# Performance work log

Measured on AMD Instinct MI355X. Metric: run time of the kernel, lower is better.

The kernel has to match this reference:

```python
import jax, jax.numpy as jnp
import numpy as np

B, C, IMG, P = 32, 3, 224, 16
D, L, H, EXP, NCLS = 768, 12, 12, 4, 1000
NP = (IMG // P) ** 2        # 196 patches
N = NP + 1                  # 197 tokens with cls
DH = D // H                 # 64 head dim
EPS = 1e-5


def setup_inputs() -> dict:
    key = jax.random.key(0)
    ks = iter(jax.random.split(key, 32))
    s = 0.02
    return {
        "img": jax.random.normal(next(ks), (B, C, IMG, IMG), jnp.float32),
        "patch_w": jax.random.normal(next(ks), (D, C * P * P), jnp.float32) * s,
        "patch_b": jnp.zeros((D,), jnp.float32),
        "cls_token": jax.random.normal(next(ks), (D,), jnp.float32) * s,
        "pos_emb": jax.random.normal(next(ks), (N, D), jnp.float32) * s,
        "ln1_w": jnp.ones((L, D), jnp.float32),
        "ln1_b": jnp.zeros((L, D), jnp.float32),
        "qkv_w": jax.random.normal(next(ks), (L, 3 * D, D), jnp.float32) * s,
        "qkv_b": jnp.zeros((L, 3 * D), jnp.float32),
        "proj_w": jax.random.normal(next(ks), (L, D, D), jnp.float32) * s,
        "proj_b": jnp.zeros((L, D), jnp.float32),
        "ln2_w": jnp.ones((L, D), jnp.float32),
        "ln2_b": jnp.zeros((L, D), jnp.float32),
        "ff1_w": jax.random.normal(next(ks), (L, EXP * D, D), jnp.float32) * s,
        "ff1_b": jnp.zeros((L, EXP * D), jnp.float32),
        "ff2_w": jax.random.normal(next(ks), (L, D, EXP * D), jnp.float32) * s,
        "ff2_b": jnp.zeros((L, D), jnp.float32),
        "head1_w": jax.random.normal(next(ks), (EXP * D, D), jnp.float32) * s,
        "head1_b": jnp.zeros((EXP * D,), jnp.float32),
        "head2_w": jax.random.normal(next(ks), (NCLS, EXP * D), jnp.float32) * s,
        "head2_b": jnp.zeros((NCLS,), jnp.float32),
    }


def _ln(x, w, b):
    m = x.mean(-1, keepdims=True)
    v = ((x - m) ** 2).mean(-1, keepdims=True)
    return (x - m) * jax.lax.rsqrt(v + EPS) * w + b


def _vit(img, patch_w, patch_b, cls_token, pos_emb, ln1_w, ln1_b, qkv_w, qkv_b,
         proj_w, proj_b, ln2_w, ln2_b, ff1_w, ff1_b, ff2_w, ff2_b,
         head1_w, head1_b, head2_w, head2_b):
    b = img.shape[0]
    g = IMG // P
    # Rearrange 'b c (h p1) (w p2) -> b (h w) (p1 p2 c)'
    x = img.reshape(b, C, g, P, g, P)
    x = x.transpose(0, 2, 4, 3, 5, 1).reshape(b, g * g, P * P * C)
    tokens = x @ patch_w.T + patch_b                           # [B, NP, D]
    cls = jnp.broadcast_to(cls_token, (b, 1, D))
    tokens = jnp.concatenate([cls, tokens], axis=1) + pos_emb  # [B, N, D]

    scale = DH ** -0.5

    def block(x, p):
        l1w, l1b, qw, qb, pw, pb, l2w, l2b, f1w, f1b, f2w, f2b = p
        h = _ln(x, l1w, l1b)
        qkv = h @ qw.T + qb                                    # [B, N, 3D]
        # '(h d qkv)' factorization: heads outermost, qkv innermost
        qkv = qkv.reshape(b, N, H, DH, 3).transpose(4, 0, 2, 1, 3)
        q, k, v = qkv[0], qkv[1], qkv[2]                       # [B, H, N, DH]
        scores = jnp.einsum('bhqd,bhkd->bhqk', q, k) * scale
        attn = jnp.einsum('bhqk,bhkd->bhqd', jax.nn.softmax(scores, axis=-1), v)
        attn = attn.transpose(0, 2, 1, 3).reshape(b, N, D)
        x = x + attn @ pw.T + pb
        h = _ln(x, l2w, l2b)
        h = jax.nn.gelu(h @ f1w.T + f1b, approximate=False)
        x = x + h @ f2w.T + f2b
        return x, None

    params = (ln1_w, ln1_b, qkv_w, qkv_b, proj_w, proj_b,
              ln2_w, ln2_b, ff1_w, ff1_b, ff2_w, ff2_b)
    tokens, _ = jax.lax.scan(block, tokens, params)

    latent = tokens[:, 0]                                      # [B, D]
    h = jnp.tanh(latent @ head1_w.T + head1_b)
    return h @ head2_w.T + head2_b                             # [B, NCLS]


def reference(img, patch_w, patch_b, cls_token, pos_emb, ln1_w, ln1_b, qkv_w,
              qkv_b, proj_w, proj_b, ln2_w, ln2_b, ff1_w, ff1_b, ff2_w, ff2_b,
              head1_w, head1_b, head2_w, head2_b):
    return _vit(img, patch_w, patch_b, cls_token, pos_emb, ln1_w, ln1_b,
                qkv_w, qkv_b, proj_w, proj_b, ln2_w, ln2_b, ff1_w, ff1_b,
                ff2_w, ff2_b, head1_w, head1_b, head2_w, head2_b)
```

## Files before the change

### kernel.cpp

```cpp
#include <hip/hip_runtime.h>
#include <math.h>

typedef unsigned short u16;
using bf16x8 = __attribute__((ext_vector_type(8))) short;
using f32x4  = __attribute__((ext_vector_type(4))) float;

#define DEV __device__ __forceinline__

constexpr int Bc = 32, Cc = 3, IMGc = 224, Pc = 16, Dc = 768, Lc = 12, Hc = 12, NCLSc = 1000;
constexpr int NPc = 196, Nc = 197, DHc = 64;
constexpr int M0 = Bc * Nc;
constexpr int MP = 6400;
constexpr int MPATCH = Bc * NPc;
constexpr int NKP = 224;
constexpr int NB = Bc * Hc;

DEV u16 f2b(float f) { union { float f; unsigned u; } c; c.f = f; unsigned r = c.u + 0x7fffu + ((c.u >> 16) & 1u); return (u16)(r >> 16); }
DEV float b2f(u16 b) { union { float f; unsigned u; } c; c.u = ((unsigned)b) << 16; return c.f; }

DEV float wsum(float v) {
#pragma unroll
  for (int m = 32; m >= 1; m >>= 1) v += __shfl_xor(v, m, 64);
  return v;
}
DEV float wmax(float v) {
#pragma unroll
  for (int m = 32; m >= 1; m >>= 1) v = fmaxf(v, __shfl_xor(v, m, 64));
  return v;
}

DEV void load_lds16(const u16* g, u16* l) {
  __builtin_amdgcn_global_load_lds((const __attribute__((address_space(1))) void*)g,
                                   (__attribute__((address_space(3))) void*)l, 16, 0, 0);
}


__global__ void cvt_kern(const float* __restrict__ in, u16* __restrict__ out, long n4) {
  long i = (long)blockIdx.x * 256 + threadIdx.x;
  if (i >= n4) return;
  float4 v = ((const float4*)in)[i];
  ushort4 r;
  r.x = f2b(v.x); r.y = f2b(v.y); r.z = f2b(v.z); r.w = f2b(v.w);
  ((ushort4*)out)[i] = r;
}

__global__ void patchify_kern(const float* __restrict__ img, u16* __restrict__ Xp) {
  int i = blockIdx.x * 256 + threadIdx.x;
  if (i >= MPATCH * Dc) return;
  int r = i / Dc, f = i - r * Dc;
  int b = r / NPc, g = r - b * NPc;
  int gi = g / 14, gj = g - gi * 14;
  int c = f % 3, t2 = f / 3;
  int pj = t2 & 15, pi = t2 >> 4;
  float v = img[(((long)(b * 3 + c) * 224) + gi * 16 + pi) * 224 + gj * 16 + pj];
  Xp[i] = f2b(v);
}

__global__ void addpos_kern(float* __restrict__ x, const float* __restrict__ cls, const float* __restrict__ pos) {
  int i = blockIdx.x * 256 + threadIdx.x;
  if (i >= M0 * 192) return;
  int row = i / 192, q = i - row * 192;
  int n = row % Nc;
  float4 p = ((const float4*)pos)[n * 192 + q];
  float4* dst = (float4*)x + (long)row * 192 + q;
  if (n == 0) {
    float4 cv = ((const float4*)cls)[q];
    float4 o; o.x = cv.x + p.x; o.y = cv.y + p.y; o.z = cv.z + p.z; o.w = cv.w + p.w;
    *dst = o;
  } else {
    float4 o = *dst;
    o.x += p.x; o.y += p.y; o.z += p.z; o.w += p.w;
    *dst = o;
  }
}

__global__ __launch_bounds__(256) void ln_kern(const float* __restrict__ x, const float* __restrict__ w,
                                               const float* __restrict__ b, u16* __restrict__ out, int rows) {
  int wid = threadIdx.x >> 6, l = threadIdx.x & 63;
  int row = blockIdx.x * 4 + wid;
  if (row >= rows) return;
  const float4* xr = (const float4*)(x + (long)row * Dc);
  float4 v[3];
#pragma unroll
  for (int i = 0; i < 3; ++i) v[i] = xr[i * 64 + l];
  float s = 0;
#pragma unroll
  for (int i = 0; i < 3; ++i) s += v[i].x + v[i].y + v[i].z + v[i].w;
  s = wsum(s);
  float mean = s * (1.0f / Dc);
  float ss = 0;
#pragma unroll
  for (int i = 0; i < 3; ++i) {
    float a0 = v[i].x - mean, a1 = v[i].y - mean, a2 = v[i].z - mean, a3 = v[i].w - mean;
    ss += a0 * a0 + a1 * a1 + a2 * a2 + a3 * a3;
  }
  ss = wsum(ss);
  float rs = rsqrtf(ss * (1.0f / Dc) + 1e-5f);
  const float4* w4 = (const float4*)w;
  const float4* b4 = (const float4*)b;
#pragma unroll
  for (int i = 0; i < 3; ++i) {
    int pos = i * 64 + l;
    float4 wv = w4[pos], bv = b4[pos];
    ushort4 o;
    o.x = f2b((v[i].x - mean) * rs * wv.x + bv.x);
    o.y = f2b((v[i].y - mean) * rs * wv.y + bv.y);
    o.z = f2b((v[i].z - mean) * rs * wv.z + bv.z);
    o.w = f2b((v[i].w - mean) * rs * wv.w + bv.w);
    ((ushort4*)out)[(long)row * 192 + pos] = o;
  }
}

__global__ __launch_bounds__(256) void softmax_kern(u16* __restrict__ S) {
  int wid = threadIdx.x >> 6, l = threadIdx.x & 63;
  int q = blockIdx.x * 4 + wid;
  if (q >= Nc) return;
  int z = blockIdx.y;
  u16* rowp = S + ((long)z * NKP + q) * NKP;
  float vals[4];
  float mx = -1e30f;
#pragma unroll
  for (int i = 0; i < 4; ++i) {
    int col = i * 64 + l;
    float vv = (col < Nc) ? b2f(rowp[col]) : -1e30f;
    vals[i] = vv;
    mx = fmaxf(mx, vv);
  }
  mx = wmax(mx);
  float sum = 0;
#pragma unroll
  for (int i = 0; i < 4; ++i) {
    int col = i * 64 + l;
    float e = (col < Nc) ? expf(vals[i] - mx) : 0.f;
    vals[i] = e;
    sum += e;
  }
  sum = wsum(sum);
  float inv = 1.0f / sum;
#pragma unroll
  for (int i = 0; i < 4; ++i) {
    int col = i * 64 + l;
    if (col < NKP) rowp[col] = (col < Nc) ? f2b(vals[i] * inv) : (u16)0;
  }
}

__global__ void latent_kern(const float* __restrict__ x, u16* __restrict__ lat) {
  int i = blockIdx.x * 256 + threadIdx.x;
  if (i >= Bc * Dc) return;
  int b = i / Dc, d = i - b * Dc;
  lat[i] = f2b(x[(long)(b * Nc) * Dc + d]);
}


enum { EPI_F32 = 0, EPI_PATCH, EPI_BF16, EPI_PV, EPI_RES, EPI_GELU, EPI_TANH, EPI_QKV };

struct GP {
  const u16* A; const u16* W;
  int lda, ldb, ldc;
  long sA, sW, sC;
  int K;
  int Aclamp, Wclamp;
  int Mv, Nv;
  float alpha;
  const float* bias;
  float* Cf; u16* Cb;
  u16 *q, *k, *v;
};

template <int EPI>
__global__ __launch_bounds__(256) void gemm_bt(GP p) {
  __shared__ alignas(16) u16 As[128 * 32];
  __shared__ alignas(16) u16 Ws[128 * 32];
  const int z = blockIdx.z;
  const u16* Ab = p.A + (long)z * p.sA;
  const u16* Wb = p.W + (long)z * p.sW;
  const int tid = threadIdx.x;
  const int l = tid & 63, wid = tid >> 6;
  const int quad = l >> 4, lr = l & 15;
  const int wr = wid >> 1, wc = wid & 1;
  const int tm = blockIdx.y * 128, tn = blockIdx.x * 128;

  f32x4 acc[4][4];
  f32x4 z4 = {0.f, 0.f, 0.f, 0.f};
#pragma unroll
  for (int i = 0; i < 4; ++i)
#pragma unroll
    for (int j = 0; j < 4; ++j) acc[i][j] = z4;

  const int sr = tid >> 2;
  const int sc = (tid & 3) * 8;
  const int ar0 = min(tm + sr, p.Aclamp - 1);
  const int ar1 = min(tm + 64 + sr, p.Aclamp - 1);
  const int wrr0 = min(tn + sr, p.Wclamp - 1);
  const int wrr1 = min(tn + 64 + sr, p.Wclamp - 1);
  const u16* a0 = Ab + (long)ar0 * p.lda + sc;
  const u16* a1 = Ab + (long)ar1 * p.lda + sc;
  const u16* w0 = Wb + (long)wrr0 * p.ldb + sc;
  const u16* w1 = Wb + (long)wrr1 * p.ldb + sc;

  for (int k0 = 0; k0 < p.K; k0 += 32) {
    load_lds16(a0 + k0, &As[tid * 8]);
    load_lds16(a1 + k0, &As[2048 + tid * 8]);
    load_lds16(w0 + k0, &Ws[tid * 8]);
    load_lds16(w1 + k0, &Ws[2048 + tid * 8]);
    __syncthreads();
    bf16x8 af[4], wf[4];
#pragma unroll
    for (int mi = 0; mi < 4; ++mi) af[mi] = *(const bf16x8*)&As[(wr * 64 + mi * 16 + lr) * 32 + quad * 8];
#pragma unroll
    for (int ni = 0; ni < 4; ++ni) wf[ni] = *(const bf16x8*)&Ws[(wc * 64 + ni * 16 + lr) * 32 + quad * 8];
#pragma unroll
    for (int mi = 0; mi < 4; ++mi)
#pragma unroll
      for (int ni = 0; ni < 4; ++ni)
        acc[mi][ni] = __builtin_amdgcn_mfma_f32_16x16x32_bf16(af[mi], wf[ni], acc[mi][ni], 0, 0, 0);
    __syncthreads();
  }

  if constexpr (EPI == EPI_QKV) {
    int hh[4], dh[4], ss[4]; float bv[4];
#pragma unroll
    for (int ni = 0; ni < 4; ++ni) {
      int col = tn + wc * 64 + ni * 16 + lr;
      hh[ni] = col / 192;
      int rem = col - hh[ni] * 192;
      dh[ni] = rem / 3;
      ss[ni] = rem - 3 * dh[ni];
      bv[ni] = p.bias[col];
    }
#pragma unroll
    for (int mi = 0; mi < 4; ++mi)
#pragma unroll
      for (int j = 0; j < 4; ++j) {
        int row = tm + wr * 64 + mi * 16 + quad * 4 + j;
        if (row >= p.Mv) continue;
        int b = row / Nc, n = row - Nc * b;
#pragma unroll
        for (int ni = 0; ni < 4; ++ni) {
          float val = acc[mi][ni][j] + bv[ni];
          if (ss[ni] == 0) {
            val *= p.alpha;
            p.q[(((long)(b * Hc + hh[ni])) * Nc + n) * DHc + dh[ni]] = f2b(val);
          } else if (ss[ni] == 1) {
            p.k[(((long)(b * Hc + hh[ni])) * Nc + n) * DHc + dh[ni]] = f2b(val);
          } else {
            p.v[(((long)(b * Hc + hh[ni])) * DHc + dh[ni]) * NKP + n] = f2b(val);
          }
        }
      }
  } else {
#pragma unroll
    for (int mi = 0; mi < 4; ++mi)
#pragma unroll
      for (int j = 0; j < 4; ++j) {
        int row = tm + wr * 64 + mi * 16 + quad * 4 + j;
        if (row >= p.Mv) continue;
#pragma unroll
        for (int ni = 0; ni < 4; ++ni) {
          int col = tn + wc * 64 + ni * 16 + lr;
          if (col >= p.Nv) continue;
          float val = acc[mi][ni][j];
          if constexpr (EPI == EPI_F32) {
            p.Cf[(long)z * p.sC + (long)row * p.ldc + col] = val + p.bias[col];
          }
          if constexpr (EPI == EPI_PATCH) {
            int b = row / NPc, t = row - NPc * b;
            p.Cf[((long)(b * Nc + 1 + t)) * p.ldc + col] = val + p.bias[col];
          }
          if constexpr (EPI == EPI_BF16) {
            p.Cb[(long)z * p.sC + (long)row * p.ldc + col] = f2b(val);
          }
          if constexpr (EPI == EPI_PV) {
            long off = (long)(z / Hc) * (Nc * Dc) + (long)(z % Hc) * DHc;
            p.Cb[off + (long)row * Dc + col] = f2b(val);
          }
          if constexpr (EPI == EPI_RES) {
            long ix = (long)row * p.ldc + col;
            p.Cf[ix] += val + p.bias[col];
          }
          if constexpr (EPI == EPI_GELU) {
            float t2 = val + p.bias[col];
            p.Cb[(long)row * p.ldc + col] = f2b(0.5f * t2 * (1.0f + erff(t2 * 0.70710678118f)));
          }
          if constexpr (EPI == EPI_TANH) {
            float t2 = val + p.bias[col];
            p.Cb[(long)row * p.ldc + col] = f2b(tanhf(t2));
          }
        }
      }
  }
}


static void cvt(const float* in, u16* out, long n, hipStream_t s) {
  long n4 = n / 4;
  cvt_kern<<<dim3((unsigned)((n4 + 255) / 256)), dim3(256), 0, s>>>(in, out, n4);
}

extern "C" void kernel_launch(void* const* d_in, const int* in_sizes, int n_in,
                              void* d_out, int out_size, void* d_ws, size_t ws_size,
                              hipStream_t stream) {
  const float* img     = (const float*)d_in[0];
  const float* patch_w = (const float*)d_in[1];
  const float* patch_b = (const float*)d_in[2];
  const float* cls_tok = (const float*)d_in[3];
  const float* pos_emb = (const float*)d_in[4];
  const float* ln1_w   = (const float*)d_in[5];
  const float* ln1_b   = (const float*)d_in[6];
  const float* qkv_w   = (const float*)d_in[7];
  const float* qkv_b   = (const float*)d_in[8];
  const float* proj_w  = (const float*)d_in[9];
  const float* proj_b  = (const float*)d_in[10];
  const float* ln2_w   = (const float*)d_in[11];
  const float* ln2_b   = (const float*)d_in[12];
  const float* ff1_w   = (const float*)d_in[13];
  const float* ff1_b   = (const float*)d_in[14];
  const float* ff2_w   = (const float*)d_in[15];
  const float* ff2_b   = (const float*)d_in[16];
  const float* h1_w    = (const float*)d_in[17];
  const float* h1_b    = (const float*)d_in[18];
  const float* h2_w    = (const float*)d_in[19];
  const float* h2_b    = (const float*)d_in[20];
  float* out = (float*)d_out;

  char* ws = (char*)d_ws;
  auto alloc = [&](long bytes) { char* p = ws; ws += (bytes + 255) & ~255L; return p; };
  u16* Wq  = (u16*)alloc(2304L * 768 * 2);
  u16* Wp  = (u16*)alloc(768L * 768 * 2);
  u16* Wf1 = (u16*)alloc(3072L * 768 * 2);
  u16* Wf2 = (u16*)alloc(768L * 3072 * 2);
  u16* Wpa = (u16*)alloc(768L * 768 * 2);
  u16* Wh1 = (u16*)alloc(3072L * 768 * 2);
  u16* Wh2 = (u16*)alloc(1000L * 3072 * 2);
  u16* Xp  = (u16*)alloc((long)MPATCH * Dc * 2);
  float* x = (float*)alloc((long)MP * Dc * 4);
  u16* hb  = (u16*)alloc((long)MP * Dc * 2);
  u16* qb  = (u16*)alloc((long)NB * Nc * DHc * 2);
  u16* kb  = (u16*)alloc((long)NB * Nc * DHc * 2);
  u16* vt  = (u16*)alloc((long)NB * DHc * NKP * 2);
  u16* S   = (u16*)alloc((long)NB * NKP * NKP * 2);
  u16* ao  = (u16*)alloc((long)MP * Dc * 2);
  u16* gb  = (u16*)alloc((long)MP * 3072 * 2);
  u16* lat = (u16*)alloc(Bc * 768L * 2);
  u16* tb  = (u16*)alloc(Bc * 3072L * 2);
  if ((size_t)(ws - (char*)d_ws) > ws_size) return;

  cvt(patch_w, Wpa, 768L * 768, stream);
  cvt(h1_w, Wh1, 3072L * 768, stream);
  cvt(h2_w, Wh2, 1000L * 3072, stream);

  patchify_kern<<<dim3((MPATCH * Dc + 255) / 256), dim3(256), 0, stream>>>(img, Xp);
  {
    GP p{};
    p.A = Xp; p.W = Wpa; p.lda = 768; p.ldb = 768; p.ldc = 768;
    p.K = 768; p.Aclamp = MPATCH; p.Wclamp = 768; p.Mv = MPATCH; p.Nv = 768;
    p.bias = patch_b; p.Cf = x;
    gemm_bt<EPI_PATCH><<<dim3(6, 49, 1), 256, 0, stream>>>(p);
  }
  addpos_kern<<<dim3((M0 * 192 + 255) / 256), dim3(256), 0, stream>>>(x, cls_tok, pos_emb);

  for (int layer = 0; layer < Lc; ++layer) {
    cvt(qkv_w + (long)layer * 2304 * 768, Wq, 2304L * 768, stream);
    cvt(proj_w + (long)layer * 768 * 768, Wp, 768L * 768, stream);
    cvt(ff1_w + (long)layer * 3072 * 768, Wf1, 3072L * 768, stream);
    cvt(ff2_w + (long)layer * 768 * 3072, Wf2, 768L * 3072, stream);

    ln_kern<<<dim3(MP / 4), 256, 0, stream>>>(x, ln1_w + layer * 768, ln1_b + layer * 768, hb, MP);

    {
      GP p{};
      p.A = hb; p.W = Wq; p.lda = 768; p.ldb = 768;
      p.K = 768; p.Aclamp = MP; p.Wclamp = 2304; p.Mv = M0; p.Nv = 2304;
      p.alpha = 0.125f; p.bias = qkv_b + layer * 2304;
      p.q = qb; p.k = kb; p.v = vt;
      gemm_bt<EPI_QKV><<<dim3(18, 50, 1), 256, 0, stream>>>(p);
    }
    {
      GP p{};
      p.A = qb; p.W = kb; p.lda = DHc; p.ldb = DHc; p.ldc = NKP;
      p.sA = (long)Nc * DHc; p.sW = (long)Nc * DHc; p.sC = (long)NKP * NKP;
      p.K = DHc; p.Aclamp = Nc; p.Wclamp = Nc; p.Mv = Nc; p.Nv = NKP;
      p.Cb = S;
      gemm_bt<EPI_BF16><<<dim3(2, 2, NB), 256, 0, stream>>>(p);
    }
    softmax_kern<<<dim3(50, NB), 256, 0, stream>>>(S);
    {
      GP p{};
      p.A = S; p.W = vt; p.lda = NKP; p.ldb = NKP;
      p.sA = (long)NKP * NKP; p.sW = (long)DHc * NKP;
      p.K = NKP; p.Aclamp = Nc; p.Wclamp = DHc; p.Mv = Nc; p.Nv = DHc;
      p.Cb = ao;
      gemm_bt<EPI_PV><<<dim3(1, 2, NB), 256, 0, stream>>>(p);
    }
    {
      GP p{};
      p.A = ao; p.W = Wp; p.lda = 768; p.ldb = 768; p.ldc = 768;
      p.K = 768; p.Aclamp = MP; p.Wclamp = 768; p.Mv = MP; p.Nv = 768;
      p.bias = proj_b + layer * 768; p.Cf = x;
      gemm_bt<EPI_RES><<<dim3(6, 50, 1), 256, 0, stream>>>(p);
    }

    ln_kern<<<dim3(MP / 4), 256, 0, stream>>>(x, ln2_w + layer * 768, ln2_b + layer * 768, hb, MP);

    {
      GP p{};
      p.A = hb; p.W = Wf1; p.lda = 768; p.ldb = 768; p.ldc = 3072;
      p.K = 768; p.Aclamp = MP; p.Wclamp = 3072; p.Mv = MP; p.Nv = 3072;
      p.bias = ff1_b + layer * 3072; p.Cb = gb;
      gemm_bt<EPI_GELU><<<dim3(24, 50, 1), 256, 0, stream>>>(p);
    }
    {
      GP p{};
      p.A = gb; p.W = Wf2; p.lda = 3072; p.ldb = 3072; p.ldc = 768;
      p.K = 3072; p.Aclamp = MP; p.Wclamp = 768; p.Mv = MP; p.Nv = 768;
      p.bias = ff2_b + layer * 768; p.Cf = x;
      gemm_bt<EPI_RES><<<dim3(6, 50, 1), 256, 0, stream>>>(p);
    }
  }

  latent_kern<<<dim3((Bc * Dc + 255) / 256), 256, 0, stream>>>(x, lat);
  {
    GP p{};
    p.A = lat; p.W = Wh1; p.lda = 768; p.ldb = 768; p.ldc = 3072;
    p.K = 768; p.Aclamp = Bc; p.Wclamp = 3072; p.Mv = Bc; p.Nv = 3072;
    p.bias = h1_b; p.Cb = tb;
    gemm_bt<EPI_TANH><<<dim3(24, 1, 1), 256, 0, stream>>>(p);
  }
  {
    GP p{};
    p.A = tb; p.W = Wh2; p.lda = 3072; p.ldb = 3072; p.ldc = 1000;
    p.K = 3072; p.Aclamp = Bc; p.Wclamp = 1000; p.Mv = Bc; p.Nv = 1000;
    p.bias = h2_b; p.Cf = out;
    gemm_bt<EPI_F32><<<dim3(8, 1, 1), 256, 0, stream>>>(p);
  }
}
```

Measured before the change: 4.932 ms.

## Double-buffer GEMM LDS tiles, XOR-swizzle LDS layout, remap workgroups per XCD

The GEMM kernel now keeps two LDS buffers and issues the next K-tile's global-to-LDS loads before computing the current tile, so memory latency overlaps with MFMA work and one barrier per iteration is dropped. The LDS column chunk is XOR-swizzled by row to reduce bank conflicts on the fragment reads. For the large GEMMs, a workgroup-ID remap groups neighbouring tiles onto the same XCD to improve L2 reuse. The cost is twice the LDS per block, which may lower occupancy.

```diff
diff --git a/kernel.cpp b/kernel.cpp
--- a/kernel.cpp
+++ b/kernel.cpp
@@ -161,6 +161,7 @@
   int K;
   int Aclamp, Wclamp;
   int Mv, Nv;
+  int swz;
   float alpha;
   const float* bias;
   float* Cf; u16* Cb;
@@ -169,8 +170,8 @@
 
 template <int EPI>
 __global__ __launch_bounds__(256) void gemm_bt(GP p) {
-  __shared__ alignas(16) u16 As[128 * 32];
-  __shared__ alignas(16) u16 Ws[128 * 32];
+  __shared__ alignas(16) u16 As[2][128 * 32];
+  __shared__ alignas(16) u16 Ws[2][128 * 32];
   const int z = blockIdx.z;
   const u16* Ab = p.A + (long)z * p.sA;
   const u16* Wb = p.W + (long)z * p.sW;
@@ -178,7 +179,21 @@
   const int l = tid & 63, wid = tid >> 6;
   const int quad = l >> 4, lr = l & 15;
   const int wr = wid >> 1, wc = wid & 1;
-  const int tm = blockIdx.y * 128, tn = blockIdx.x * 128;
+
+  int tm, tn;
+  if (p.swz) {
+    const int gx = gridDim.x;
+    const int nwg = gx * gridDim.y;
+    const int orig = blockIdx.y * gx + blockIdx.x;
+    const int q8 = nwg >> 3, r8 = nwg & 7;
+    const int xcd = orig & 7, loc = orig >> 3;
+    const int wgid = (xcd < r8 ? xcd * (q8 + 1) : r8 * (q8 + 1) + (xcd - r8) * q8) + loc;
+    tm = (wgid / gx) * 128;
+    tn = (wgid % gx) * 128;
+  } else {
+    tm = blockIdx.y * 128;
+    tn = blockIdx.x * 128;
+  }
 
   f32x4 acc[4][4];
   f32x4 z4 = {0.f, 0.f, 0.f, 0.f};
@@ -188,34 +203,52 @@
     for (int j = 0; j < 4; ++j) acc[i][j] = z4;
 
   const int sr = tid >> 2;
-  const int sc = (tid & 3) * 8;
+  const int s_sw = ((tid & 3) ^ ((sr >> 1) & 3)) * 8;
   const int ar0 = min(tm + sr, p.Aclamp - 1);
   const int ar1 = min(tm + 64 + sr, p.Aclamp - 1);
   const int wrr0 = min(tn + sr, p.Wclamp - 1);
   const int wrr1 = min(tn + 64 + sr, p.Wclamp - 1);
-  const u16* a0 = Ab + (long)ar0 * p.lda + sc;
-  const u16* a1 = Ab + (long)ar1 * p.lda + sc;
-  const u16* w0 = Wb + (long)wrr0 * p.ldb + sc;
-  const u16* w1 = Wb + (long)wrr1 * p.ldb + sc;
-
-  for (int k0 = 0; k0 < p.K; k0 += 32) {
-    load_lds16(a0 + k0, &As[tid * 8]);
-    load_lds16(a1 + k0, &As[2048 + tid * 8]);
-    load_lds16(w0 + k0, &Ws[tid * 8]);
-    load_lds16(w1 + k0, &Ws[2048 + tid * 8]);
-    __syncthreads();
+  const u16* a0 = Ab + (long)ar0 * p.lda + s_sw;
+  const u16* a1 = Ab + (long)ar1 * p.lda + s_sw;
+  const u16* w0 = Wb + (long)wrr0 * p.ldb + s_sw;
+  const u16* w1 = Wb + (long)wrr1 * p.ldb + s_sw;
+
+#define STAGE(buf, k0)                                  \
+  do {                                                  \
+    load_lds16(a0 + (k0), &As[buf][tid * 8]);           \
+    load_lds16(a1 + (k0), &As[buf][2048 + tid * 8]);    \
+    load_lds16(w0 + (k0), &Ws[buf][tid * 8]);           \
+    load_lds16(w1 + (k0), &Ws[buf][2048 + tid * 8]);    \
+  } while (0)
+
+  const int nt = p.K >> 5;
+  STAGE(0, 0);
+  __syncthreads();
+  int cur = 0;
+  for (int t = 0; t < nt; ++t) {
+    if (t + 1 < nt) STAGE(cur ^ 1, (t + 1) * 32);
     bf16x8 af[4], wf[4];
 #pragma unroll
-    for (int mi = 0; mi < 4; ++mi) af[mi] = *(const bf16x8*)&As[(wr * 64 + mi * 16 + lr) * 32 + quad * 8];
-#pragma unroll
-    for (int ni = 0; ni < 4; ++ni) wf[ni] = *(const bf16x8*)&Ws[(wc * 64 + ni * 16 + lr) * 32 + quad * 8];
+    for (int mi = 0; mi < 4; ++mi) {
+      const int R = wr * 64 + mi * 16 + lr;
+      const int qq = quad ^ ((R >> 1) & 3);
+      af[mi] = *(const bf16x8*)((const char*)As[cur] + R * 64 + (qq << 4));
+    }
+#pragma unroll
+    for (int ni = 0; ni < 4; ++ni) {
+      const int R = wc * 64 + ni * 16 + lr;
+      const int qq = quad ^ ((R >> 1) & 3);
+      wf[ni] = *(const bf16x8*)((const char*)Ws[cur] + R * 64 + (qq << 4));
+    }
 #pragma unroll
     for (int mi = 0; mi < 4; ++mi)
 #pragma unroll
       for (int ni = 0; ni < 4; ++ni)
         acc[mi][ni] = __builtin_amdgcn_mfma_f32_16x16x32_bf16(af[mi], wf[ni], acc[mi][ni], 0, 0, 0);
     __syncthreads();
-  }
+    cur ^= 1;
+  }
+#undef STAGE
 
   if constexpr (EPI == EPI_QKV) {
     int hh[4], dh[4], ss[4]; float bv[4];
@@ -354,7 +387,7 @@
     GP p{};
     p.A = Xp; p.W = Wpa; p.lda = 768; p.ldb = 768; p.ldc = 768;
     p.K = 768; p.Aclamp = MPATCH; p.Wclamp = 768; p.Mv = MPATCH; p.Nv = 768;
-    p.bias = patch_b; p.Cf = x;
+    p.swz = 1; p.bias = patch_b; p.Cf = x;
     gemm_bt<EPI_PATCH><<<dim3(6, 49, 1), 256, 0, stream>>>(p);
   }
   addpos_kern<<<dim3((M0 * 192 + 255) / 256), dim3(256), 0, stream>>>(x, cls_tok, pos_emb);
@@ -371,7 +404,7 @@
       GP p{};
       p.A = hb; p.W = Wq; p.lda = 768; p.ldb = 768;
       p.K = 768; p.Aclamp = MP; p.Wclamp = 2304; p.Mv = M0; p.Nv = 2304;
-      p.alpha = 0.125f; p.bias = qkv_b + layer * 2304;
+      p.swz = 1; p.alpha = 0.125f; p.bias = qkv_b + layer * 2304;
       p.q = qb; p.k = kb; p.v = vt;
       gemm_bt<EPI_QKV><<<dim3(18, 50, 1), 256, 0, stream>>>(p);
     }
@@ -396,7 +429,7 @@
       GP p{};
       p.A = ao; p.W = Wp; p.lda = 768; p.ldb = 768; p.ldc = 768;
       p.K = 768; p.Aclamp = MP; p.Wclamp = 768; p.Mv = MP; p.Nv = 768;
-      p.bias = proj_b + layer * 768; p.Cf = x;
+      p.swz = 1; p.bias = proj_b + layer * 768; p.Cf = x;
       gemm_bt<EPI_RES><<<dim3(6, 50, 1), 256, 0, stream>>>(p);
     }
 
@@ -406,14 +439,14 @@
       GP p{};
       p.A = hb; p.W = Wf1; p.lda = 768; p.ldb = 768; p.ldc = 3072;
       p.K = 768; p.Aclamp = MP; p.Wclamp = 3072; p.Mv = MP; p.Nv = 3072;
-      p.bias = ff1_b + layer * 3072; p.Cb = gb;
+      p.swz = 1; p.bias = ff1_b + layer * 3072; p.Cb = gb;
       gemm_bt<EPI_GELU><<<dim3(24, 50, 1), 256, 0, stream>>>(p);
     }
     {
       GP p{};
       p.A = gb; p.W = Wf2; p.lda = 3072; p.ldb = 3072; p.ldc = 768;
       p.K = 3072; p.Aclamp = MP; p.Wclamp = 768; p.Mv = MP; p.Nv = 768;
-      p.bias = ff2_b + layer * 768; p.Cf = x;
+      p.swz = 1; p.bias = ff2_b + layer * 768; p.Cf = x;
       gemm_bt<EPI_RES><<<dim3(6, 50, 1), 256, 0, stream>>>(p);
     }
   }
@@ -423,14 +456,14 @@
     GP p{};
     p.A = lat; p.W = Wh1; p.lda = 768; p.ldb = 768; p.ldc = 3072;
     p.K = 768; p.Aclamp = Bc; p.Wclamp = 3072; p.Mv = Bc; p.Nv = 3072;
-    p.bias = h1_b; p.Cb = tb;
+    p.swz = 1; p.bias = h1_b; p.Cb = tb;
     gemm_bt<EPI_TANH><<<dim3(24, 1, 1), 256, 0, stream>>>(p);
   }
   {
     GP p{};
     p.A = tb; p.W = Wh2; p.lda = 3072; p.ldb = 3072; p.ldc = 1000;
     p.K = 3072; p.Aclamp = Bc; p.Wclamp = 1000; p.Mv = Bc; p.Nv = 1000;
-    p.bias = h2_b; p.Cf = out;
+    p.swz = 1; p.bias = h2_b; p.Cf = out;
     gemm_bt<EPI_F32><<<dim3(8, 1, 1), 256, 0, stream>>>(p);
   }
 }
```

After: 4.572 ms. 7.3% less time.
